# Optimization experiments

Measured on AMD Instinct MI355X. Metric: run time of the kernel, lower is better.

Reference implementation:

```python
import jax, jax.numpy as jnp
import numpy as np

AVG_NOBJ = 49.0
NEG_SLOPE = 0.01  # torch leaky_relu default


def eops_1_to_2(x, nobj, aggregation):
    """x: [B,N,C] -> [B,C,5,N,N] equivariant basis (rank-1 -> rank-2)."""
    B, N, C = x.shape
    xt = jnp.transpose(x, (0, 2, 1))  # B,C,N
    if aggregation == 'sum':
        agg = xt.sum(-1) / AVG_NOBJ                      # B,C
    elif aggregation == 'mean':
        agg = xt.sum(-1) / nobj[:, None]                 # B,C
    elif aggregation == 'max':
        agg = xt.max(-1)
    elif aggregation == 'min':
        agg = xt.min(-1)
    eye = jnp.eye(N, dtype=x.dtype)                      # N,N
    op1 = xt[:, :, :, None] * eye                        # x_i on diagonal
    op2 = jnp.broadcast_to(xt[:, :, None, :], (B, C, N, N))  # x_j along rows
    op3 = jnp.broadcast_to(xt[:, :, :, None], (B, C, N, N))  # x_i along cols
    op4 = agg[:, :, None, None] * eye                    # agg on diagonal
    op5 = jnp.broadcast_to(agg[:, :, None, None], (B, C, N, N))  # agg everywhere
    return jnp.stack([op1, op2, op3, op4, op5], axis=2)  # B,C,5,N,N


def setup_inputs() -> dict:
    key = jax.random.key(0)
    k1, k2 = jax.random.split(key)
    B, N, C, S = 8, 128, 64, 64
    basis_total = 5 * 4  # 5 basis ops per config char, config='smxn'
    inputs = jax.random.normal(k1, (B, N, C), dtype=jnp.float32)
    mask = jnp.ones((B, N, N, 1), dtype=jnp.float32)
    nobj = jnp.full((B,), 100.0, dtype=jnp.float32)
    coefs = jax.random.normal(k2, (C, S, basis_total), dtype=jnp.float32) * np.sqrt(2.0 / (C * basis_total)).astype(np.float32)
    bias = jnp.zeros((S,), dtype=jnp.float32)
    return {"inputs": inputs, "mask": mask, "nobj": nobj, "coefs": coefs, "bias": bias}


def reference(inputs, mask, nobj, coefs, bias):
    # config = 'smxn' -> sum, mean, max, min basis tensors, concat on basis axis
    ops = jnp.concatenate(
        [eops_1_to_2(inputs, nobj, a) for a in ('sum', 'mean', 'max', 'min')],
        axis=2)  # B,C,20,N,N
    out = jnp.einsum('dsb,ndbij->nijs', coefs, ops)      # B,N,N,S
    out = out + bias[None, None, None, :]
    out = jnp.where(out >= 0, out, NEG_SLOPE * out)      # leaky_relu
    return out * mask
```

## Files before the change

kernel.cpp:

```cpp
#include <hip/hip_runtime.h>

constexpr int N = 128, S = 64;
constexpr float INV_AVG = 1.0f / 49.0f;
constexpr float SLOPE = 0.01f;

typedef float f4 __attribute__((ext_vector_type(4)));

constexpr int WS_BASE = 0;
constexpr int WS_DIAG = 65536;
constexpr int WS_R    = 131072;

__global__ __launch_bounds__(256) void prep_kernel(
    const float* __restrict__ x,
    const float* __restrict__ nobj,
    const float* __restrict__ coefs,
    const float* __restrict__ bias,
    float* __restrict__ ws)
{
  __shared__ float xs[8192];
  __shared__ float ag[256];
  __shared__ float part[3584];

  const int tid = threadIdx.x;
  const int n   = blockIdx.x >> 5;
  const int i0  = (blockIdx.x & 31) << 2;

  {
    const float4* xg = (const float4*)(x + n * N * 64);
    float4* xs4 = (float4*)xs;
#pragma unroll
    for (int k = 0; k < 8; ++k) xs4[tid + k * 256] = xg[tid + k * 256];
  }
  __syncthreads();

  {
    const int d = tid & 63, grp = tid >> 6;
    float sm = 0.f, mx = -INFINITY, mn = INFINITY;
    for (int i = grp * 32; i < grp * 32 + 32; ++i) {
      float v = xs[i * 64 + d];
      sm += v; mx = fmaxf(mx, v); mn = fminf(mn, v);
    }
    part[grp * 64 + d]       = sm;
    part[256 + grp * 64 + d] = mx;
    part[512 + grp * 64 + d] = mn;
  }
  __syncthreads();
  if (tid < 64) {
    float s0 = part[tid] + part[64 + tid] + part[128 + tid] + part[192 + tid];
    float m0 = fmaxf(fmaxf(part[256 + tid], part[320 + tid]),
                     fmaxf(part[384 + tid], part[448 + tid]));
    float n0 = fminf(fminf(part[512 + tid], part[576 + tid]),
                     fminf(part[640 + tid], part[704 + tid]));
    ag[tid]       = s0 * INV_AVG;
    ag[64 + tid]  = s0 / nobj[n];
    ag[128 + tid] = m0;
    ag[192 + tid] = n0;
  }
  __syncthreads();

  {
    const int g = tid >> 6;
    const int s = tid & 63;
    float pA[4] = {0,0,0,0}, pR[4] = {0,0,0,0}, pC[4] = {0,0,0,0};
    float pD = 0.f, pE = 0.f;
#pragma unroll
    for (int k = 0; k < 16; ++k) {
      const int e = k * 256 + tid;
      const int d = e >> 6;
      const float4* cp = (const float4*)(coefs + e * 20);
      float4 f0 = cp[0], f1 = cp[1], f2 = cp[2], f3 = cp[3], f4v = cp[4];
      float w1v = f0.x + f1.y + f2.z + f3.w;
      float w2v = f0.y + f1.z + f2.w + f4v.x;
      float w3v = f0.z + f1.w + f3.x + f4v.y;
#pragma unroll
      for (int m = 0; m < 4; ++m) {
        float xv = xs[(i0 + m) * 64 + d];
        pA[m] += xv * w1v;
        pR[m] += xv * w2v;
        pC[m] += xv * w3v;
      }
      pD += ag[d] * f0.w + ag[64 + d] * f2.x + ag[128 + d] * f3.y + ag[192 + d] * f4v.z;
      pE += ag[d] * f1.x + ag[64 + d] * f2.y + ag[128 + d] * f3.z + ag[192 + d] * f4v.w;
    }
#pragma unroll
    for (int m = 0; m < 4; ++m) {
      part[m * 256 + g * 64 + s]        = pA[m];
      part[(4 + m) * 256 + g * 64 + s]  = pC[m];
      part[(8 + m) * 256 + g * 64 + s]  = pR[m];
    }
    part[3072 + g * 64 + s] = pD;
    part[3328 + g * 64 + s] = pE;
  }
  __syncthreads();

  if (tid < 64) {
    const int s = tid;
    float D = part[3072 + s] + part[3072 + 64 + s]
            + part[3072 + 128 + s] + part[3072 + 192 + s];
    float E = part[3328 + s] + part[3328 + 64 + s]
            + part[3328 + 128 + s] + part[3328 + 192 + s];
    float bv = bias[s];
#pragma unroll
    for (int m = 0; m < 4; ++m) {
      float A = part[m * 256 + s] + part[m * 256 + 64 + s]
              + part[m * 256 + 128 + s] + part[m * 256 + 192 + s];
      float C = part[(4 + m) * 256 + s] + part[(4 + m) * 256 + 64 + s]
              + part[(4 + m) * 256 + 128 + s] + part[(4 + m) * 256 + 192 + s];
      float R = part[(8 + m) * 256 + s] + part[(8 + m) * 256 + 64 + s]
              + part[(8 + m) * 256 + 128 + s] + part[(8 + m) * 256 + 192 + s];
      const int o = (n * N + i0 + m) * 64 + s;
      ws[WS_BASE + o] = C + E + bv;
      ws[WS_DIAG + o] = A + D;
      ws[WS_R    + o] = R;
    }
  }
}

__global__ __launch_bounds__(256) void assemble_kernel(
    const float* __restrict__ ws,
    const float* __restrict__ mask,
    float* __restrict__ out)
{
  const int g  = blockIdx.x * 256 + threadIdx.x;
  const int l  = g & 15;
  const int p  = g >> 4;
  const int j  = p & 127;
  const int bi = p >> 7;
  const int i  = bi & 127;
  const int n  = bi >> 7;

  const float4* B4 = (const float4*)(ws + WS_BASE);
  const float4* G4 = (const float4*)(ws + WS_DIAG);
  const float4* R4 = (const float4*)(ws + WS_R);

  float4 b = B4[bi * 16 + l];
  float4 r = R4[(n * N + j) * 16 + l];
  float mk = mask[p];

  float v0 = b.x + r.x;
  float v1 = b.y + r.y;
  float v2 = b.z + r.z;
  float v3 = b.w + r.w;
  if (i == j) {
    float4 dg = G4[bi * 16 + l];
    v0 += dg.x; v1 += dg.y; v2 += dg.z; v3 += dg.w;
  }
  v0 = (v0 >= 0.f) ? v0 : SLOPE * v0;
  v1 = (v1 >= 0.f) ? v1 : SLOPE * v1;
  v2 = (v2 >= 0.f) ? v2 : SLOPE * v2;
  v3 = (v3 >= 0.f) ? v3 : SLOPE * v3;

  f4 o;
  o.x = v0 * mk; o.y = v1 * mk; o.z = v2 * mk; o.w = v3 * mk;
  __builtin_nontemporal_store(o, &((f4*)out)[g]);
}

extern "C" void kernel_launch(void* const* d_in, const int* in_sizes, int n_in,
                              void* d_out, int out_size, void* d_ws, size_t ws_size,
                              hipStream_t stream) {
  const float* x     = (const float*)d_in[0];
  const float* mask  = (const float*)d_in[1];
  const float* nobj  = (const float*)d_in[2];
  const float* coefs = (const float*)d_in[3];
  const float* bias  = (const float*)d_in[4];
  float* out = (float*)d_out;
  float* ws  = (float*)d_ws;

  prep_kernel<<<256, 256, 0, stream>>>(x, nobj, coefs, bias, ws);
  assemble_kernel<<<8192, 256, 0, stream>>>(ws, mask, out);
}
```

Baseline: 83.82 us.

## Fuse prep and assemble into one kernel with per-block LDS recomputation

Merges the two kernels into one 512-thread kernel. Each block computes the row-broadcast term R for all j of its batch directly in LDS, then writes its output rows. This removes the workspace round trip and the second launch. In exchange every block recomputes R redundantly, and the kernel uses one block per CU with plain (not nontemporal) stores. The LDS rows are padded to reduce bank conflicts.

After: 95.59 us. +14.0%, slower.

```diff
diff --git a/kernel.cpp b/kernel.cpp
--- a/kernel.cpp
+++ b/kernel.cpp
@@ -1,56 +1,71 @@
 #include <hip/hip_runtime.h>
 
-constexpr int N = 128, S = 64;
+constexpr int N = 128;
 constexpr float INV_AVG = 1.0f / 49.0f;
 constexpr float SLOPE = 0.01f;
+constexpr int XP = 68;
 
-typedef float f4 __attribute__((ext_vector_type(4)));
+constexpr int O_XS   = 0;
+constexpr int O_W2   = O_XS + 128 * XP;
+constexpr int O_R    = O_W2 + 4096;
+constexpr int O_PART = O_R + 8192;
+constexpr int O_AG   = O_PART + 5120;
+constexpr int O_BV   = O_AG + 256;
+constexpr int O_DV   = O_BV + 256;
+constexpr int LDS_F  = O_DV + 256;
 
-constexpr int WS_BASE = 0;
-constexpr int WS_DIAG = 65536;
-constexpr int WS_R    = 131072;
-
-__global__ __launch_bounds__(256) void prep_kernel(
+__global__ __launch_bounds__(512, 1) void fused_kernel(
     const float* __restrict__ x,
+    const float* __restrict__ mask,
     const float* __restrict__ nobj,
     const float* __restrict__ coefs,
     const float* __restrict__ bias,
-    float* __restrict__ ws)
+    float* __restrict__ out)
 {
-  __shared__ float xs[8192];
-  __shared__ float ag[256];
-  __shared__ float part[3584];
+  __shared__ __align__(16) float lds[LDS_F];
+  float* xs    = lds + O_XS;
+  float* w2s   = lds + O_W2;
+  float* Rr    = lds + O_R;
+  float* part  = lds + O_PART;
+  float* ag    = lds + O_AG;
+  float* basev = lds + O_BV;
+  float* diagv = lds + O_DV;
 
   const int tid = threadIdx.x;
   const int n   = blockIdx.x >> 5;
   const int i0  = (blockIdx.x & 31) << 2;
 
   {
-    const float4* xg = (const float4*)(x + n * N * 64);
-    float4* xs4 = (float4*)xs;
+    const float4* xg = (const float4*)(x + (size_t)n * N * 64);
 #pragma unroll
-    for (int k = 0; k < 8; ++k) xs4[tid + k * 256] = xg[tid + k * 256];
+    for (int q = 0; q < 4; ++q) {
+      const int idx = q * 512 + tid;
+      const int j = idx >> 4, c = idx & 15;
+      *(float4*)(xs + j * XP + c * 4) = xg[idx];
+    }
   }
   __syncthreads();
 
   {
     const int d = tid & 63, grp = tid >> 6;
     float sm = 0.f, mx = -INFINITY, mn = INFINITY;
-    for (int i = grp * 32; i < grp * 32 + 32; ++i) {
-      float v = xs[i * 64 + d];
+    for (int i = grp * 16; i < grp * 16 + 16; ++i) {
+      float v = xs[i * XP + d];
       sm += v; mx = fmaxf(mx, v); mn = fminf(mn, v);
     }
-    part[grp * 64 + d]       = sm;
-    part[256 + grp * 64 + d] = mx;
-    part[512 + grp * 64 + d] = mn;
+    part[grp * 64 + d]        = sm;
+    part[512 + grp * 64 + d]  = mx;
+    part[1024 + grp * 64 + d] = mn;
   }
   __syncthreads();
   if (tid < 64) {
-    float s0 = part[tid] + part[64 + tid] + part[128 + tid] + part[192 + tid];
-    float m0 = fmaxf(fmaxf(part[256 + tid], part[320 + tid]),
-                     fmaxf(part[384 + tid], part[448 + tid]));
-    float n0 = fminf(fminf(part[512 + tid], part[576 + tid]),
-                     fminf(part[640 + tid], part[704 + tid]));
+    float s0 = 0.f, m0 = -INFINITY, n0 = INFINITY;
+#pragma unroll
+    for (int g = 0; g < 8; ++g) {
+      s0 += part[g * 64 + tid];
+      m0 = fmaxf(m0, part[512 + g * 64 + tid]);
+      n0 = fminf(n0, part[1024 + g * 64 + tid]);
+    }
     ag[tid]       = s0 * INV_AVG;
     ag[64 + tid]  = s0 / nobj[n];
     ag[128 + tid] = m0;
@@ -61,22 +76,22 @@
   {
     const int g = tid >> 6;
     const int s = tid & 63;
-    float pA[4] = {0,0,0,0}, pR[4] = {0,0,0,0}, pC[4] = {0,0,0,0};
+    float pA[4] = {0,0,0,0}, pC[4] = {0,0,0,0};
     float pD = 0.f, pE = 0.f;
 #pragma unroll
-    for (int k = 0; k < 16; ++k) {
-      const int e = k * 256 + tid;
-      const int d = e >> 6;
-      const float4* cp = (const float4*)(coefs + e * 20);
+    for (int k = 0; k < 8; ++k) {
+      const int e = k * 512 + tid;
+      const int d = k * 8 + g;
+      const float4* cp = (const float4*)(coefs + (size_t)e * 20);
       float4 f0 = cp[0], f1 = cp[1], f2 = cp[2], f3 = cp[3], f4v = cp[4];
       float w1v = f0.x + f1.y + f2.z + f3.w;
       float w2v = f0.y + f1.z + f2.w + f4v.x;
       float w3v = f0.z + f1.w + f3.x + f4v.y;
+      w2s[e] = w2v;
 #pragma unroll
       for (int m = 0; m < 4; ++m) {
-        float xv = xs[(i0 + m) * 64 + d];
+        float xv = xs[(i0 + m) * XP + d];
         pA[m] += xv * w1v;
-        pR[m] += xv * w2v;
         pC[m] += xv * w3v;
       }
       pD += ag[d] * f0.w + ag[64 + d] * f2.x + ag[128 + d] * f3.y + ag[192 + d] * f4v.z;
@@ -84,75 +99,85 @@
     }
 #pragma unroll
     for (int m = 0; m < 4; ++m) {
-      part[m * 256 + g * 64 + s]        = pA[m];
-      part[(4 + m) * 256 + g * 64 + s]  = pC[m];
-      part[(8 + m) * 256 + g * 64 + s]  = pR[m];
+      part[m * 512 + g * 64 + s]       = pA[m];
+      part[(4 + m) * 512 + g * 64 + s] = pC[m];
     }
-    part[3072 + g * 64 + s] = pD;
-    part[3328 + g * 64 + s] = pE;
+    part[8 * 512 + g * 64 + s] = pD;
+    part[9 * 512 + g * 64 + s] = pE;
   }
   __syncthreads();
 
-  if (tid < 64) {
-    const int s = tid;
-    float D = part[3072 + s] + part[3072 + 64 + s]
-            + part[3072 + 128 + s] + part[3072 + 192 + s];
-    float E = part[3328 + s] + part[3328 + 64 + s]
-            + part[3328 + 128 + s] + part[3328 + 192 + s];
-    float bv = bias[s];
+  {
+    const int s4 = tid & 15;
+    const int j0 = (tid >> 4) * 4;
+    const float4* w2q = (const float4*)w2s;
+    float4 acc[4];
 #pragma unroll
-    for (int m = 0; m < 4; ++m) {
-      float A = part[m * 256 + s] + part[m * 256 + 64 + s]
-              + part[m * 256 + 128 + s] + part[m * 256 + 192 + s];
-      float C = part[(4 + m) * 256 + s] + part[(4 + m) * 256 + 64 + s]
-              + part[(4 + m) * 256 + 128 + s] + part[(4 + m) * 256 + 192 + s];
-      float R = part[(8 + m) * 256 + s] + part[(8 + m) * 256 + 64 + s]
-              + part[(8 + m) * 256 + 128 + s] + part[(8 + m) * 256 + 192 + s];
-      const int o = (n * N + i0 + m) * 64 + s;
-      ws[WS_BASE + o] = C + E + bv;
-      ws[WS_DIAG + o] = A + D;
-      ws[WS_R    + o] = R;
+    for (int jj = 0; jj < 4; ++jj) { acc[jj].x = acc[jj].y = acc[jj].z = acc[jj].w = 0.f; }
+#pragma unroll
+    for (int d0 = 0; d0 < 16; ++d0) {
+      float4 w0 = w2q[(d0 * 4 + 0) * 16 + s4];
+      float4 w1 = w2q[(d0 * 4 + 1) * 16 + s4];
+      float4 w2 = w2q[(d0 * 4 + 2) * 16 + s4];
+      float4 w3 = w2q[(d0 * 4 + 3) * 16 + s4];
+#pragma unroll
+      for (int jj = 0; jj < 4; ++jj) {
+        float4 xv = *(const float4*)(xs + (j0 + jj) * XP + d0 * 4);
+        acc[jj].x += xv.x * w0.x + xv.y * w1.x + xv.z * w2.x + xv.w * w3.x;
+        acc[jj].y += xv.x * w0.y + xv.y * w1.y + xv.z * w2.y + xv.w * w3.y;
+        acc[jj].z += xv.x * w0.z + xv.y * w1.z + xv.z * w2.z + xv.w * w3.z;
+        acc[jj].w += xv.x * w0.w + xv.y * w1.w + xv.z * w2.w + xv.w * w3.w;
+      }
+    }
+#pragma unroll
+    for (int jj = 0; jj < 4; ++jj)
+      ((float4*)Rr)[(j0 + jj) * 16 + s4] = acc[jj];
+  }
+
+  if (tid < 256) {
+    const int m = tid >> 6, s = tid & 63;
+    float A = 0.f, C = 0.f, D = 0.f, E = 0.f;
+#pragma unroll
+    for (int g = 0; g < 8; ++g) {
+      A += part[m * 512 + g * 64 + s];
+      C += part[(4 + m) * 512 + g * 64 + s];
+      D += part[8 * 512 + g * 64 + s];
+      E += part[9 * 512 + g * 64 + s];
+    }
+    basev[m * 64 + s] = C + E + bias[s];
+    diagv[m * 64 + s] = A + D;
+  }
+  __syncthreads();
+
+  {
+    const float* mrow = mask + (size_t)(n * N + i0) * N;
+    float4* outq = (float4*)out + (size_t)(n * N + i0) * N * 16;
+    const float4* Rq = (const float4*)Rr;
+    const float4* bq = (const float4*)basev;
+    const float4* dq = (const float4*)diagv;
+#pragma unroll
+    for (int q = 0; q < 16; ++q) {
+      const int idx = q * 512 + tid;
+      const int l = idx & 15;
+      const int j = (idx >> 4) & 127;
+      const int m = idx >> 11;
+      float4 b = bq[m * 16 + l];
+      float4 r = Rq[j * 16 + l];
+      float mk = mrow[m * N + j];
+      float v0 = b.x + r.x, v1 = b.y + r.y, v2 = b.z + r.z, v3 = b.w + r.w;
+      if (i0 + m == j) {
+        float4 dgv = dq[m * 16 + l];
+        v0 += dgv.x; v1 += dgv.y; v2 += dgv.z; v3 += dgv.w;
+      }
+      v0 = (v0 >= 0.f) ? v0 : SLOPE * v0;
+      v1 = (v1 >= 0.f) ? v1 : SLOPE * v1;
+      v2 = (v2 >= 0.f) ? v2 : SLOPE * v2;
+      v3 = (v3 >= 0.f) ? v3 : SLOPE * v3;
+      float4 o;
+      o.x = v0 * mk; o.y = v1 * mk; o.z = v2 * mk; o.w = v3 * mk;
+      outq[idx] = o;
     }
   }
-}
-
-__global__ __launch_bounds__(256) void assemble_kernel(
-    const float* __restrict__ ws,
-    const float* __restrict__ mask,
-    float* __restrict__ out)
-{
-  const int g  = blockIdx.x * 256 + threadIdx.x;
-  const int l  = g & 15;
-  const int p  = g >> 4;
-  const int j  = p & 127;
-  const int bi = p >> 7;
-  const int i  = bi & 127;
-  const int n  = bi >> 7;
-
-  const float4* B4 = (const float4*)(ws + WS_BASE);
-  const float4* G4 = (const float4*)(ws + WS_DIAG);
-  const float4* R4 = (const float4*)(ws + WS_R);
-
-  float4 b = B4[bi * 16 + l];
-  float4 r = R4[(n * N + j) * 16 + l];
-  float mk = mask[p];
-
-  float v0 = b.x + r.x;
-  float v1 = b.y + r.y;
-  float v2 = b.z + r.z;
-  float v3 = b.w + r.w;
-  if (i == j) {
-    float4 dg = G4[bi * 16 + l];
-    v0 += dg.x; v1 += dg.y; v2 += dg.z; v3 += dg.w;
-  }
-  v0 = (v0 >= 0.f) ? v0 : SLOPE * v0;
-  v1 = (v1 >= 0.f) ? v1 : SLOPE * v1;
-  v2 = (v2 >= 0.f) ? v2 : SLOPE * v2;
-  v3 = (v3 >= 0.f) ? v3 : SLOPE * v3;
-
-  f4 o;
-  o.x = v0 * mk; o.y = v1 * mk; o.z = v2 * mk; o.w = v3 * mk;
-  __builtin_nontemporal_store(o, &((f4*)out)[g]);
 }
 
 extern "C" void kernel_launch(void* const* d_in, const int* in_sizes, int n_in,
@@ -164,8 +189,6 @@
   const float* coefs = (const float*)d_in[3];
   const float* bias  = (const float*)d_in[4];
   float* out = (float*)d_out;
-  float* ws  = (float*)d_ws;
 
-  prep_kernel<<<256, 256, 0, stream>>>(x, nobj, coefs, bias, ws);
-  assemble_kernel<<<8192, 256, 0, stream>>>(ws, mask, out);
+  fused_kernel<<<256, 512, 0, stream>>>(x, mask, nobj, coefs, bias, out);
 }
```
